# Kernel optimization log

Hardware: AMD Instinct MI355X
Metric: run time of the kernel (lower is better)

Reference implementation:

```python
import jax, jax.numpy as jnp
import numpy as np

N = 50000   # num_nodes
D = 128     # h_dim
R = 32      # num_rels * 2 (forward + inverse relations)
B = 8       # num_bases
E = 600000  # num_edges


def setup_inputs() -> dict:
    key = jax.random.key(0)
    ks = jax.random.split(key, 14)
    s = 1.0 / np.sqrt(D)
    return {
        "h_ids": jnp.arange(N, dtype=jnp.int32),
        "src": jax.random.randint(ks[0], (E,), 0, N),
        "dst": jax.random.randint(ks[1], (E,), 0, N),
        "etype": jax.random.randint(ks[2], (E,), 0, R),
        "norm": jax.random.uniform(ks[3], (E, 1), dtype=jnp.float32),
        "embedding": jax.random.normal(ks[4], (N, D), dtype=jnp.float32) * 0.05,
        "w_comp1": jax.random.normal(ks[5], (R, B), dtype=jnp.float32) * (1.0 / np.sqrt(B)),
        "bases1": jax.random.normal(ks[6], (B, D, D), dtype=jnp.float32) * s,
        "loop_w1": jax.random.normal(ks[7], (D, D), dtype=jnp.float32) * s,
        "bias1": jnp.zeros((D,), dtype=jnp.float32),
        "w_comp2": jax.random.normal(ks[8], (R, B), dtype=jnp.float32) * (1.0 / np.sqrt(B)),
        "bases2": jax.random.normal(ks[9], (B, D, D), dtype=jnp.float32) * s,
        "loop_w2": jax.random.normal(ks[10], (D, D), dtype=jnp.float32) * s,
        "bias2": jnp.zeros((D,), dtype=jnp.float32),
    }


def _rel_graph_conv(h, src, dst, etype, norm, w_comp, bases, loop_w, bias, act):
    # basis decomposition: W[r] = sum_b w_comp[r,b] * bases[b]
    W = jnp.einsum('rb,bio->rio', w_comp, bases)          # [R, D, D]
    # transform every node by every relation weight (dense GEMM)
    all_t = jnp.einsum('ni,rio->nro', h, W)               # [N, R, D]
    # per-edge gather of relation-specific transformed source features
    msg = all_t[src, etype] * norm                        # [E, D]
    # scatter-aggregate messages at destination nodes
    agg = jax.ops.segment_sum(msg, dst, num_segments=h.shape[0])  # [N, D]
    out = agg + h @ loop_w + bias                         # self-loop + bias
    return act(out) if act is not None else out


def reference(h_ids, src, dst, etype, norm, embedding,
              w_comp1, bases1, loop_w1, bias1,
              w_comp2, bases2, loop_w2, bias2):
    # EmbeddingLayer
    h = embedding[h_ids]                                  # [N, D]
    # hidden layer 0: relu activation (idx < num_hidden_layers-1)
    h = _rel_graph_conv(h, src, dst, etype, norm, w_comp1, bases1, loop_w1, bias1, jax.nn.relu)
    # hidden layer 1: no activation (last layer)
    h = _rel_graph_conv(h, src, dst, etype, norm, w_comp2, bases2, loop_w2, bias2, None)
    return h
```

## Files before the change

### kernel.cpp

```cpp
#include <hip/hip_runtime.h>

#define DD 128
#define NB 8
#define KTOT 1152

typedef unsigned int uint_t;
typedef __attribute__((ext_vector_type(8))) _Float16 half8v;
typedef __attribute__((ext_vector_type(2))) _Float16 half2v;
typedef __attribute__((ext_vector_type(4))) float f32x4;

static __device__ __forceinline__ void gld_lds16(const _Float16* g, _Float16* l)
{
  __builtin_amdgcn_global_load_lds(
      (const __attribute__((address_space(1))) void*)g,
      (__attribute__((address_space(3))) void*)l, 16, 0, 0);
}

static __device__ __forceinline__ half2v bc_h2(uint_t u)
{
  union { uint_t u; half2v h; } c; c.u = u; return c.h;
}

static __device__ __forceinline__ float fdot2(uint_t a, uint_t b, float acc)
{
#if __has_builtin(__builtin_amdgcn_fdot2)
  return __builtin_amdgcn_fdot2(bc_h2(a), bc_h2(b), acc, false);
#else
  half2v x = bc_h2(a), y = bc_h2(b);
  return acc + (float)x[0] * (float)y[0] + (float)x[1] * (float)y[1];
#endif
}

__global__ __launch_bounds__(256) void k_prep_w(
    const float* __restrict__ bases1, const float* __restrict__ loopw1,
    const float* __restrict__ bases2, const float* __restrict__ loopw2,
    _Float16* __restrict__ WcA)
{
  int i = blockIdx.x * 256 + threadIdx.x;
  if (i >= 2 * 36 * DD * 32) return;
  int layer = i / (36 * DD * 32);
  int rem   = i % (36 * DD * 32);
  int ks    = rem / (DD * 32);
  int rem2  = rem % (DD * 32);
  int feat  = rem2 / 32;
  int j     = rem2 % 32;
  int k     = ks * 32 + j;
  const float* basesL = layer ? bases2 : bases1;
  const float* loopwL = layer ? loopw2 : loopw1;
  float v;
  if (k < 1024) {
    int kk = k >> 3, b = k & 7;
    v = basesL[((size_t)b * DD + kk) * DD + feat];
  } else {
    v = loopwL[(size_t)(k - 1024) * DD + feat];
  }
  WcA[i] = (_Float16)v;
}

__global__ __launch_bounds__(256) void k_cast(
    const float* __restrict__ h, const int* __restrict__ ids,
    _Float16* __restrict__ hf, int N)
{
  int i = blockIdx.x * 256 + threadIdx.x;
  if (i >= N * (DD / 8)) return;
  int n  = i / (DD / 8);
  int k8 = (i % (DD / 8)) * 8;
  int row = ids ? ids[n] : n;
  const float* hp = h + (size_t)row * DD + k8;
  float4 v0 = *(const float4*)hp;
  float4 v1 = *(const float4*)(hp + 4);
  union { _Float16 e[8]; uint4 q; } p;
  p.e[0]=(_Float16)v0.x; p.e[1]=(_Float16)v0.y; p.e[2]=(_Float16)v0.z; p.e[3]=(_Float16)v0.w;
  p.e[4]=(_Float16)v1.x; p.e[5]=(_Float16)v1.y; p.e[6]=(_Float16)v1.z; p.e[7]=(_Float16)v1.w;
  *(uint4*)&hf[(size_t)n * DD + k8] = p.q;
}

__global__ __launch_bounds__(256) void k_zero(int* __restrict__ p, int n)
{
  int i = blockIdx.x * 256 + threadIdx.x;
  if (i < n) p[i] = 0;
}

__global__ __launch_bounds__(256) void k_hist(
    const int* __restrict__ dst, int* __restrict__ cnt, int E)
{
  int e = blockIdx.x * 256 + threadIdx.x;
  if (e < E) atomicAdd(&cnt[dst[e]], 1);
}

__global__ __launch_bounds__(256) void k_bsum(
    const int* __restrict__ cnt, int* __restrict__ bsum, int N)
{
  __shared__ int s[256];
  int i = blockIdx.x * 256 + threadIdx.x;
  s[threadIdx.x] = (i < N) ? ((cnt[i] + 1) & ~1) : 0;
  __syncthreads();
  for (int off = 128; off > 0; off >>= 1) {
    if (threadIdx.x < off) s[threadIdx.x] += s[threadIdx.x + off];
    __syncthreads();
  }
  if (threadIdx.x == 0) bsum[blockIdx.x] = s[0];
}

__global__ __launch_bounds__(256) void k_scanb(
    const int* __restrict__ bsum, int* __restrict__ boff, int nb)
{
  __shared__ int s[256];
  int t = threadIdx.x;
  int own = (t < nb) ? bsum[t] : 0;
  s[t] = own;
  __syncthreads();
  for (int off = 1; off < 256; off <<= 1) {
    int v = (t >= off) ? s[t - off] : 0;
    __syncthreads();
    s[t] += v;
    __syncthreads();
  }
  if (t < nb) boff[t] = s[t] - own;
}

__global__ __launch_bounds__(256) void k_scan3(
    const int* __restrict__ cnt, const int* __restrict__ boff,
    int* __restrict__ row_start, int* __restrict__ psrc, int N)
{
  __shared__ int s[256];
  int t = threadIdx.x;
  int i = blockIdx.x * 256 + t;
  int c = (i < N) ? cnt[i] : 0;
  int v = (c + 1) & ~1;
  s[t] = v;
  __syncthreads();
  for (int off = 1; off < 256; off <<= 1) {
    int u = (t >= off) ? s[t - off] : 0;
    __syncthreads();
    s[t] += u;
    __syncthreads();
  }
  if (i < N) {
    int rs = boff[blockIdx.x] + s[t] - v;
    row_start[i] = rs;
    if (c & 1) psrc[rs + c] = 0;
  }
}

__global__ __launch_bounds__(256) void k_place(
    const int* __restrict__ dst, const int* __restrict__ src,
    const int* __restrict__ etype, const float* __restrict__ norm,
    const int* __restrict__ row_start, int* __restrict__ cursor,
    int* __restrict__ psrc, int2* __restrict__ en, int E)
{
  int e = blockIdx.x * 256 + threadIdx.x;
  if (e < E) {
    int v = dst[e];
    int slot = row_start[v] + atomicAdd(&cursor[v], 1);
    psrc[slot] = src[e];
    en[slot] = make_int2(etype[e], __float_as_int(norm[e]));
  }
}

__global__ __launch_bounds__(256) void k_payload_pair(
    const int2* __restrict__ en,
    const float* __restrict__ wcomp1, const float* __restrict__ wcomp2,
    _Float16* __restrict__ c1, _Float16* __restrict__ c2, int npair)
{
  int i = blockIdx.x * 256 + threadIdx.x;
  if (i >= npair) return;
  int2 e0 = en[2 * i], e1 = en[2 * i + 1];
  float n0 = __int_as_float(e0.y), n1 = __int_as_float(e1.y);
  const float* w10 = wcomp1 + e0.x * NB;
  const float* w11 = wcomp1 + e1.x * NB;
  const float* w20 = wcomp2 + e0.x * NB;
  const float* w21 = wcomp2 + e1.x * NB;

  union { _Float16 h[16]; uint4 q[2]; } p;
  #pragma unroll
  for (int b = 0; b < NB; b++) {
    p.h[b * 2]     = (_Float16)(w10[b] * n0);
    p.h[b * 2 + 1] = (_Float16)(w11[b] * n1);
  }
  *(uint4*)&c1[(size_t)i * 16]     = p.q[0];
  *(uint4*)&c1[(size_t)i * 16 + 8] = p.q[1];
  #pragma unroll
  for (int b = 0; b < NB; b++) {
    p.h[b * 2]     = (_Float16)(w20[b] * n0);
    p.h[b * 2 + 1] = (_Float16)(w21[b] * n1);
  }
  *(uint4*)&c2[(size_t)i * 16]     = p.q[0];
  *(uint4*)&c2[(size_t)i * 16 + 8] = p.q[1];
}

__global__ __launch_bounds__(256) void k_agg(
    const int* __restrict__ rowst, const int* __restrict__ cnt,
    const int* __restrict__ psrc, const _Float16* __restrict__ cpair,
    const _Float16* __restrict__ hf,
    _Float16* __restrict__ agg, int N)
{
  int v = blockIdx.x * 4 + (threadIdx.x >> 6);
  if (v >= N) return;
  int lane = threadIdx.x & 63;
  const uint_t* hf32 = (const uint_t*)hf;
  const int beg = rowst[v];
  const int npairs = (cnt[v] + 1) >> 1;
  const uint_t* cp = (const uint_t*)cpair + (size_t)(beg >> 1) * 8;
  const int* ps = psrc + beg;

  float ax[NB] = {}, ay[NB] = {};
  int i = 0;
  for (; i + 4 <= npairs; i += 4) {
    uint_t u[8], lo[4], hi[4];
    #pragma unroll
    for (int q = 0; q < 8; q++)
      u[q] = hf32[(size_t)ps[2*i + q] * 64 + lane];
    #pragma unroll
    for (int q = 0; q < 4; q++) {
      lo[q] = __builtin_amdgcn_perm(u[2*q], u[2*q+1], 0x01000504);
      hi[q] = __builtin_amdgcn_perm(u[2*q], u[2*q+1], 0x03020706);
    }
    #pragma unroll
    for (int b = 0; b < NB; b++) {
      #pragma unroll
      for (int q = 0; q < 4; q++) {
        uint_t cc = cp[(size_t)(i + q) * 8 + b];
        ax[b] = fdot2(cc, lo[q], ax[b]);
        ay[b] = fdot2(cc, hi[q], ay[b]);
      }
    }
  }
  for (; i + 2 <= npairs; i += 2) {
    int s0 = ps[2*i + 0], s1 = ps[2*i + 1];
    int s2 = ps[2*i + 2], s3 = ps[2*i + 3];
    uint_t u0 = hf32[(size_t)s0 * 64 + lane];
    uint_t u1 = hf32[(size_t)s1 * 64 + lane];
    uint_t u2 = hf32[(size_t)s2 * 64 + lane];
    uint_t u3 = hf32[(size_t)s3 * 64 + lane];
    uint_t lo01 = __builtin_amdgcn_perm(u0, u1, 0x01000504);
    uint_t hi01 = __builtin_amdgcn_perm(u0, u1, 0x03020706);
    uint_t lo23 = __builtin_amdgcn_perm(u2, u3, 0x01000504);
    uint_t hi23 = __builtin_amdgcn_perm(u2, u3, 0x03020706);
    #pragma unroll
    for (int b = 0; b < NB; b++) {
      uint_t ca = cp[(size_t)i * 8 + b];
      uint_t cb = cp[(size_t)(i + 1) * 8 + b];
      ax[b] = fdot2(ca, lo01, ax[b]);
      ay[b] = fdot2(ca, hi01, ay[b]);
      ax[b] = fdot2(cb, lo23, ax[b]);
      ay[b] = fdot2(cb, hi23, ay[b]);
    }
  }
  if (i < npairs) {
    int s0 = ps[2*i + 0], s1 = ps[2*i + 1];
    uint_t u0 = hf32[(size_t)s0 * 64 + lane];
    uint_t u1 = hf32[(size_t)s1 * 64 + lane];
    uint_t lo01 = __builtin_amdgcn_perm(u0, u1, 0x01000504);
    uint_t hi01 = __builtin_amdgcn_perm(u0, u1, 0x03020706);
    #pragma unroll
    for (int b = 0; b < NB; b++) {
      uint_t ca = cp[(size_t)i * 8 + b];
      ax[b] = fdot2(ca, lo01, ax[b]);
      ay[b] = fdot2(ca, hi01, ay[b]);
    }
  }

  union { _Float16 e[8]; uint4 q; } p0, p1;
  #pragma unroll
  for (int b = 0; b < NB; b++) { p0.e[b] = (_Float16)ax[b]; p1.e[b] = (_Float16)ay[b]; }
  uint4* dstp = (uint4*)&agg[(size_t)v * 1024 + lane * 16];
  dstp[0] = p0.q;
  dstp[1] = p1.q;
}

template <int LAYER>
__global__ __launch_bounds__(256) void k_mm(
    const _Float16* __restrict__ agg,
    const _Float16* __restrict__ hf,
    const _Float16* __restrict__ WcA,
    const float* __restrict__ bias,
    float* __restrict__ outf, _Float16* __restrict__ outh, int N)
{
  __shared__ _Float16 sB[2][2048];

  const int n0   = blockIdx.x * 32;
  const int wv   = threadIdx.x >> 6;
  const int lane = threadIdx.x & 63;
  const int l15  = lane & 15, l4 = lane >> 4;

  int nodeS = n0 + (lane & 31); if (nodeS >= N) nodeS = N - 1;
  const int ksl = 2 * wv + (lane >> 5);

  f32x4 acc[2][2];
  #pragma unroll
  for (int a = 0; a < 2; a++)
    #pragma unroll
    for (int b = 0; b < 2; b++) acc[a][b] = (f32x4)0.f;

  const int fbase = wv * 32 + l15;
  const int koff  = l4 * 8;

  auto STAGE = [&](int buf, int t) {
    const _Float16* g;
    if (t < 16) g = &agg[(size_t)nodeS * 1024 + t * 64 + ksl * 8];
    else        g = &hf [(size_t)nodeS * DD   + (t - 16) * 64 + ksl * 8];
    gld_lds16(g, &sB[buf][2 * wv * 256]);
  };

  auto COMPUTE = [&](int buf, int t) {
    #pragma unroll
    for (int sub = 0; sub < 2; sub++) {
      const int ks = 2 * t + sub;
      half8v af0 = *(const half8v*)&WcA[((size_t)ks * DD + fbase     ) * 32 + koff];
      half8v af1 = *(const half8v*)&WcA[((size_t)ks * DD + fbase + 16) * 32 + koff];
      half8v bf0 = *(const half8v*)&sB[buf][(sub * 4 + l4) * 256 + l15 * 8];
      half8v bf1 = *(const half8v*)&sB[buf][(sub * 4 + l4) * 256 + (16 + l15) * 8];
      acc[0][0] = __builtin_amdgcn_mfma_f32_16x16x32_f16(af0, bf0, acc[0][0], 0, 0, 0);
      acc[0][1] = __builtin_amdgcn_mfma_f32_16x16x32_f16(af0, bf1, acc[0][1], 0, 0, 0);
      acc[1][0] = __builtin_amdgcn_mfma_f32_16x16x32_f16(af1, bf0, acc[1][0], 0, 0, 0);
      acc[1][1] = __builtin_amdgcn_mfma_f32_16x16x32_f16(af1, bf1, acc[1][1], 0, 0, 0);
    }
  };

  STAGE(0, 0);
  __syncthreads();
  int cur = 0;
  for (int t = 0; t < 17; t++) {
    STAGE(cur ^ 1, t + 1);
    COMPUTE(cur, t);
    __syncthreads();
    cur ^= 1;
  }
  COMPUTE(cur, 17);

  #pragma unroll
  for (int mf = 0; mf < 2; mf++)
    #pragma unroll
    for (int nf = 0; nf < 2; nf++) {
      int n = n0 + nf * 16 + l15;
      if (n >= N) continue;
      int feat = wv * 32 + mf * 16 + l4 * 4;
      if (LAYER == 1) {
        union { _Float16 e[4]; uint2 q; } p;
        #pragma unroll
        for (int r = 0; r < 4; r++)
          p.e[r] = (_Float16)fmaxf(acc[mf][nf][r] + bias[feat + r], 0.f);
        *(uint2*)&outh[(size_t)n * DD + feat] = p.q;
      } else {
        float4 o;
        o.x = acc[mf][nf][0] + bias[feat + 0];
        o.y = acc[mf][nf][1] + bias[feat + 1];
        o.z = acc[mf][nf][2] + bias[feat + 2];
        o.w = acc[mf][nf][3] + bias[feat + 3];
        *(float4*)&outf[(size_t)n * DD + feat] = o;
      }
    }
}

extern "C" void kernel_launch(void* const* d_in, const int* in_sizes, int n_in,
                              void* d_out, int out_size, void* d_ws, size_t ws_size,
                              hipStream_t stream)
{
  const int*   h_ids     = (const int*)d_in[0];
  const int*   src       = (const int*)d_in[1];
  const int*   dst       = (const int*)d_in[2];
  const int*   etype     = (const int*)d_in[3];
  const float* norm      = (const float*)d_in[4];
  const float* embedding = (const float*)d_in[5];
  const float* w_comp1   = (const float*)d_in[6];
  const float* bases1    = (const float*)d_in[7];
  const float* loop_w1   = (const float*)d_in[8];
  const float* bias1     = (const float*)d_in[9];
  const float* w_comp2   = (const float*)d_in[10];
  const float* bases2    = (const float*)d_in[11];
  const float* loop_w2   = (const float*)d_in[12];
  const float* bias2     = (const float*)d_in[13];

  const int N = in_sizes[0];
  const int E = in_sizes[1];
  const int S = (E + N) & ~1;
  const int NPAIR = S >> 1;
  const int NBLK = (N + 255) / 256;

  char* base = (char*)d_ws;
  size_t off = 0;
  auto alloc = [&](size_t bytes) -> char* {
    char* p = base + off;
    off += (bytes + 255) & ~(size_t)255;
    return p;
  };
  _Float16* agg  = (_Float16*)alloc((size_t)N * 1024 * 2);
  _Float16* hfp  = (_Float16*)alloc((size_t)N * DD * 2);
  _Float16* h1h  = (_Float16*)alloc((size_t)N * DD * 2);
  _Float16* WcA  = (_Float16*)alloc((size_t)2 * 36 * DD * 32 * 2);
  int*      cnt    = (int*)   alloc((size_t)2 * N * 4);
  int*      cursor = cnt + N;
  int2*     en     = (int2*)  alloc((size_t)S * 8);
  int*      rowst  = (int*)   alloc((size_t)N * 4);
  int*      bsum   = (int*)   alloc(256 * 4);
  int*      boff   = (int*)   alloc(256 * 4);
  int*      psrc   = (int*)   alloc((size_t)S * 4);
  _Float16* c1     = (_Float16*)alloc((size_t)S * 8 * 2);
  _Float16* c2     = (_Float16*)alloc((size_t)S * 8 * 2);
  float*    out    = (float*)d_out;

  int zn = (int)(((char*)(en + S) - (char*)cnt) / 4);
  k_zero <<<(zn + 255) / 256, 256, 0, stream>>>(cnt, zn);
  k_hist <<<(E + 255) / 256, 256, 0, stream>>>(dst, cnt, E);
  k_bsum <<<NBLK, 256, 0, stream>>>(cnt, bsum, N);
  k_scanb<<<1, 256, 0, stream>>>(bsum, boff, NBLK);
  k_scan3<<<NBLK, 256, 0, stream>>>(cnt, boff, rowst, psrc, N);
  k_place<<<(E + 255) / 256, 256, 0, stream>>>(dst, src, etype, norm,
                                               rowst, cursor, psrc, en, E);
  k_payload_pair<<<(NPAIR + 255) / 256, 256, 0, stream>>>(
      en, w_comp1, w_comp2, c1, c2, NPAIR);

  k_prep_w<<<(2 * 36 * DD * 32 + 255) / 256, 256, 0, stream>>>(bases1, loop_w1, bases2, loop_w2, WcA);

  dim3 gmm((N + 31) / 32);
  int gagg = (N + 3) / 4;

  k_cast<<<(N * (DD / 8) + 255) / 256, 256, 0, stream>>>(embedding, h_ids, hfp, N);
  k_agg<<<gagg, 256, 0, stream>>>(rowst, cnt, psrc, c1, hfp, agg, N);
  k_mm<1><<<gmm, 256, 0, stream>>>(agg, hfp, WcA, bias1, nullptr, h1h, N);

  k_agg<<<gagg, 256, 0, stream>>>(rowst, cnt, psrc, c2, h1h, agg, N);
  k_mm<2><<<gmm, 256, 0, stream>>>(agg, h1h, WcA + (size_t)36 * DD * 32, bias2, out, nullptr, N);
}
```

Measured before the change: 289.4 us.

## Fuse per-basis aggregation and MFMA projection into one kernel per layer

Merges the edge-aggregation kernel and the MFMA GEMM kernel so each block of 16 nodes aggregates its per-basis features straight into a swizzled LDS tile, appends the self-loop features, and then runs the 36-step MFMA reduction from LDS. This removes the N x 1024 fp16 intermediate buffer round trip through global memory and two launches. In exchange, tiles shrink from 32 to 16 nodes, the weight fragments are reloaded per 16-node block, double-buffered async staging is dropped, and each block's GEMM waits on its slowest node's aggregation.

```diff
diff --git a/kernel.cpp b/kernel.cpp
--- a/kernel.cpp
+++ b/kernel.cpp
@@ -8,13 +8,6 @@
 typedef __attribute__((ext_vector_type(8))) _Float16 half8v;
 typedef __attribute__((ext_vector_type(2))) _Float16 half2v;
 typedef __attribute__((ext_vector_type(4))) float f32x4;
-
-static __device__ __forceinline__ void gld_lds16(const _Float16* g, _Float16* l)
-{
-  __builtin_amdgcn_global_load_lds(
-      (const __attribute__((address_space(1))) void*)g,
-      (__attribute__((address_space(3))) void*)l, 16, 0, 0);
-}
 
 static __device__ __forceinline__ half2v bc_h2(uint_t u)
 {
@@ -189,168 +182,134 @@
   *(uint4*)&c2[(size_t)i * 16 + 8] = p.q[1];
 }
 
-__global__ __launch_bounds__(256) void k_agg(
+template <int LAYER>
+__global__ __launch_bounds__(256) void k_fused(
     const int* __restrict__ rowst, const int* __restrict__ cnt,
     const int* __restrict__ psrc, const _Float16* __restrict__ cpair,
-    const _Float16* __restrict__ hf,
-    _Float16* __restrict__ agg, int N)
-{
-  int v = blockIdx.x * 4 + (threadIdx.x >> 6);
-  if (v >= N) return;
-  int lane = threadIdx.x & 63;
-  const uint_t* hf32 = (const uint_t*)hf;
-  const int beg = rowst[v];
-  const int npairs = (cnt[v] + 1) >> 1;
-  const uint_t* cp = (const uint_t*)cpair + (size_t)(beg >> 1) * 8;
-  const int* ps = psrc + beg;
-
-  float ax[NB] = {}, ay[NB] = {};
-  int i = 0;
-  for (; i + 4 <= npairs; i += 4) {
-    uint_t u[8], lo[4], hi[4];
-    #pragma unroll
-    for (int q = 0; q < 8; q++)
-      u[q] = hf32[(size_t)ps[2*i + q] * 64 + lane];
-    #pragma unroll
-    for (int q = 0; q < 4; q++) {
-      lo[q] = __builtin_amdgcn_perm(u[2*q], u[2*q+1], 0x01000504);
-      hi[q] = __builtin_amdgcn_perm(u[2*q], u[2*q+1], 0x03020706);
-    }
-    #pragma unroll
-    for (int b = 0; b < NB; b++) {
-      #pragma unroll
-      for (int q = 0; q < 4; q++) {
-        uint_t cc = cp[(size_t)(i + q) * 8 + b];
-        ax[b] = fdot2(cc, lo[q], ax[b]);
-        ay[b] = fdot2(cc, hi[q], ay[b]);
-      }
-    }
-  }
-  for (; i + 2 <= npairs; i += 2) {
-    int s0 = ps[2*i + 0], s1 = ps[2*i + 1];
-    int s2 = ps[2*i + 2], s3 = ps[2*i + 3];
-    uint_t u0 = hf32[(size_t)s0 * 64 + lane];
-    uint_t u1 = hf32[(size_t)s1 * 64 + lane];
-    uint_t u2 = hf32[(size_t)s2 * 64 + lane];
-    uint_t u3 = hf32[(size_t)s3 * 64 + lane];
-    uint_t lo01 = __builtin_amdgcn_perm(u0, u1, 0x01000504);
-    uint_t hi01 = __builtin_amdgcn_perm(u0, u1, 0x03020706);
-    uint_t lo23 = __builtin_amdgcn_perm(u2, u3, 0x01000504);
-    uint_t hi23 = __builtin_amdgcn_perm(u2, u3, 0x03020706);
-    #pragma unroll
-    for (int b = 0; b < NB; b++) {
-      uint_t ca = cp[(size_t)i * 8 + b];
-      uint_t cb = cp[(size_t)(i + 1) * 8 + b];
-      ax[b] = fdot2(ca, lo01, ax[b]);
-      ay[b] = fdot2(ca, hi01, ay[b]);
-      ax[b] = fdot2(cb, lo23, ax[b]);
-      ay[b] = fdot2(cb, hi23, ay[b]);
-    }
-  }
-  if (i < npairs) {
-    int s0 = ps[2*i + 0], s1 = ps[2*i + 1];
-    uint_t u0 = hf32[(size_t)s0 * 64 + lane];
-    uint_t u1 = hf32[(size_t)s1 * 64 + lane];
-    uint_t lo01 = __builtin_amdgcn_perm(u0, u1, 0x01000504);
-    uint_t hi01 = __builtin_amdgcn_perm(u0, u1, 0x03020706);
-    #pragma unroll
-    for (int b = 0; b < NB; b++) {
-      uint_t ca = cp[(size_t)i * 8 + b];
-      ax[b] = fdot2(ca, lo01, ax[b]);
-      ay[b] = fdot2(ca, hi01, ay[b]);
-    }
-  }
-
-  union { _Float16 e[8]; uint4 q; } p0, p1;
-  #pragma unroll
-  for (int b = 0; b < NB; b++) { p0.e[b] = (_Float16)ax[b]; p1.e[b] = (_Float16)ay[b]; }
-  uint4* dstp = (uint4*)&agg[(size_t)v * 1024 + lane * 16];
-  dstp[0] = p0.q;
-  dstp[1] = p1.q;
-}
-
-template <int LAYER>
-__global__ __launch_bounds__(256) void k_mm(
-    const _Float16* __restrict__ agg,
     const _Float16* __restrict__ hf,
     const _Float16* __restrict__ WcA,
     const float* __restrict__ bias,
     float* __restrict__ outf, _Float16* __restrict__ outh, int N)
 {
-  __shared__ _Float16 sB[2][2048];
-
-  const int n0   = blockIdx.x * 32;
+  __shared__ _Float16 sB[144 * 16 * 8];
+
+  const int n0   = blockIdx.x * 16;
   const int wv   = threadIdx.x >> 6;
   const int lane = threadIdx.x & 63;
   const int l15  = lane & 15, l4 = lane >> 4;
-
-  int nodeS = n0 + (lane & 31); if (nodeS >= N) nodeS = N - 1;
-  const int ksl = 2 * wv + (lane >> 5);
-
-  f32x4 acc[2][2];
-  #pragma unroll
-  for (int a = 0; a < 2; a++)
+  const uint_t* hf32 = (const uint_t*)hf;
+
+  for (int r = wv; r < 16; r += 4) {
+    int v = n0 + r;
+    if (v >= N) continue;
+    const int beg = rowst[v];
+    const int npairs = (cnt[v] + 1) >> 1;
+    const uint_t* cp = (const uint_t*)cpair + (size_t)(beg >> 1) * 8;
+    const int* ps = psrc + beg;
+
+    float ax[NB] = {}, ay[NB] = {};
+    int i = 0;
+    for (; i + 4 <= npairs; i += 4) {
+      uint_t u[8], lo[4], hi[4];
+      #pragma unroll
+      for (int q = 0; q < 8; q++)
+        u[q] = hf32[(size_t)ps[2*i + q] * 64 + lane];
+      #pragma unroll
+      for (int q = 0; q < 4; q++) {
+        lo[q] = __builtin_amdgcn_perm(u[2*q], u[2*q+1], 0x01000504);
+        hi[q] = __builtin_amdgcn_perm(u[2*q], u[2*q+1], 0x03020706);
+      }
+      #pragma unroll
+      for (int b = 0; b < NB; b++) {
+        #pragma unroll
+        for (int q = 0; q < 4; q++) {
+          uint_t cc = cp[(size_t)(i + q) * 8 + b];
+          ax[b] = fdot2(cc, lo[q], ax[b]);
+          ay[b] = fdot2(cc, hi[q], ay[b]);
+        }
+      }
+    }
+    for (; i + 2 <= npairs; i += 2) {
+      uint_t u0 = hf32[(size_t)ps[2*i + 0] * 64 + lane];
+      uint_t u1 = hf32[(size_t)ps[2*i + 1] * 64 + lane];
+      uint_t u2 = hf32[(size_t)ps[2*i + 2] * 64 + lane];
+      uint_t u3 = hf32[(size_t)ps[2*i + 3] * 64 + lane];
+      uint_t lo01 = __builtin_amdgcn_perm(u0, u1, 0x01000504);
+      uint_t hi01 = __builtin_amdgcn_perm(u0, u1, 0x03020706);
+      uint_t lo23 = __builtin_amdgcn_perm(u2, u3, 0x01000504);
+      uint_t hi23 = __builtin_amdgcn_perm(u2, u3, 0x03020706);
+      #pragma unroll
+      for (int b = 0; b < NB; b++) {
+        uint_t ca = cp[(size_t)i * 8 + b];
+        uint_t cb = cp[(size_t)(i + 1) * 8 + b];
+        ax[b] = fdot2(ca, lo01, ax[b]);
+        ay[b] = fdot2(ca, hi01, ay[b]);
+        ax[b] = fdot2(cb, lo23, ax[b]);
+        ay[b] = fdot2(cb, hi23, ay[b]);
+      }
+    }
+    if (i < npairs) {
+      uint_t u0 = hf32[(size_t)ps[2*i + 0] * 64 + lane];
+      uint_t u1 = hf32[(size_t)ps[2*i + 1] * 64 + lane];
+      uint_t lo01 = __builtin_amdgcn_perm(u0, u1, 0x01000504);
+      uint_t hi01 = __builtin_amdgcn_perm(u0, u1, 0x03020706);
+      #pragma unroll
+      for (int b = 0; b < NB; b++) {
+        uint_t ca = cp[(size_t)i * 8 + b];
+        ax[b] = fdot2(ca, lo01, ax[b]);
+        ay[b] = fdot2(ca, hi01, ay[b]);
+      }
+    }
+
+    union { _Float16 e[8]; uint4 q; } p0, p1;
     #pragma unroll
-    for (int b = 0; b < 2; b++) acc[a][b] = (f32x4)0.f;
-
+    for (int b = 0; b < NB; b++) { p0.e[b] = (_Float16)ax[b]; p1.e[b] = (_Float16)ay[b]; }
+    int c0 = 2 * lane, c1 = 2 * lane + 1;
+    *(uint4*)&sB[(c0 * 16 + ((r + c0) & 15)) * 8] = p0.q;
+    *(uint4*)&sB[(c1 * 16 + ((r + c1) & 15)) * 8] = p1.q;
+    uint_t hv = hf32[(size_t)v * 64 + lane];
+    int ch = 128 + (lane >> 5) * 8 + ((lane & 31) >> 2);
+    int jb = ((2 * lane) & 7) * 2;
+    *(uint_t*)((char*)sB + (ch * 16 + ((r + ch) & 15)) * 16 + jb) = hv;
+  }
+  __syncthreads();
+
+  f32x4 acc[2];
+  acc[0] = (f32x4)0.f; acc[1] = (f32x4)0.f;
   const int fbase = wv * 32 + l15;
   const int koff  = l4 * 8;
 
-  auto STAGE = [&](int buf, int t) {
-    const _Float16* g;
-    if (t < 16) g = &agg[(size_t)nodeS * 1024 + t * 64 + ksl * 8];
-    else        g = &hf [(size_t)nodeS * DD   + (t - 16) * 64 + ksl * 8];
-    gld_lds16(g, &sB[buf][2 * wv * 256]);
-  };
-
-  auto COMPUTE = [&](int buf, int t) {
+  #pragma unroll 6
+  for (int ks = 0; ks < 36; ks++) {
+    half8v af0 = *(const half8v*)&WcA[((size_t)ks * DD + fbase     ) * 32 + koff];
+    half8v af1 = *(const half8v*)&WcA[((size_t)ks * DD + fbase + 16) * 32 + koff];
+    int c = (ks >> 1) * 8 + (ks & 1) * 4 + l4;
+    half8v bf = *(const half8v*)&sB[(c * 16 + ((l15 + c) & 15)) * 8];
+    acc[0] = __builtin_amdgcn_mfma_f32_16x16x32_f16(af0, bf, acc[0], 0, 0, 0);
+    acc[1] = __builtin_amdgcn_mfma_f32_16x16x32_f16(af1, bf, acc[1], 0, 0, 0);
+  }
+
+  int n = n0 + l15;
+  if (n < N) {
     #pragma unroll
-    for (int sub = 0; sub < 2; sub++) {
-      const int ks = 2 * t + sub;
-      half8v af0 = *(const half8v*)&WcA[((size_t)ks * DD + fbase     ) * 32 + koff];
-      half8v af1 = *(const half8v*)&WcA[((size_t)ks * DD + fbase + 16) * 32 + koff];
-      half8v bf0 = *(const half8v*)&sB[buf][(sub * 4 + l4) * 256 + l15 * 8];
-      half8v bf1 = *(const half8v*)&sB[buf][(sub * 4 + l4) * 256 + (16 + l15) * 8];
-      acc[0][0] = __builtin_amdgcn_mfma_f32_16x16x32_f16(af0, bf0, acc[0][0], 0, 0, 0);
-      acc[0][1] = __builtin_amdgcn_mfma_f32_16x16x32_f16(af0, bf1, acc[0][1], 0, 0, 0);
-      acc[1][0] = __builtin_amdgcn_mfma_f32_16x16x32_f16(af1, bf0, acc[1][0], 0, 0, 0);
-      acc[1][1] = __builtin_amdgcn_mfma_f32_16x16x32_f16(af1, bf1, acc[1][1], 0, 0, 0);
-    }
-  };
-
-  STAGE(0, 0);
-  __syncthreads();
-  int cur = 0;
-  for (int t = 0; t < 17; t++) {
-    STAGE(cur ^ 1, t + 1);
-    COMPUTE(cur, t);
-    __syncthreads();
-    cur ^= 1;
-  }
-  COMPUTE(cur, 17);
-
-  #pragma unroll
-  for (int mf = 0; mf < 2; mf++)
-    #pragma unroll
-    for (int nf = 0; nf < 2; nf++) {
-      int n = n0 + nf * 16 + l15;
-      if (n >= N) continue;
+    for (int mf = 0; mf < 2; mf++) {
       int feat = wv * 32 + mf * 16 + l4 * 4;
       if (LAYER == 1) {
         union { _Float16 e[4]; uint2 q; } p;
         #pragma unroll
-        for (int r = 0; r < 4; r++)
-          p.e[r] = (_Float16)fmaxf(acc[mf][nf][r] + bias[feat + r], 0.f);
+        for (int rr = 0; rr < 4; rr++)
+          p.e[rr] = (_Float16)fmaxf(acc[mf][rr] + bias[feat + rr], 0.f);
         *(uint2*)&outh[(size_t)n * DD + feat] = p.q;
       } else {
         float4 o;
-        o.x = acc[mf][nf][0] + bias[feat + 0];
-        o.y = acc[mf][nf][1] + bias[feat + 1];
-        o.z = acc[mf][nf][2] + bias[feat + 2];
-        o.w = acc[mf][nf][3] + bias[feat + 3];
+        o.x = acc[mf][0] + bias[feat + 0];
+        o.y = acc[mf][1] + bias[feat + 1];
+        o.z = acc[mf][2] + bias[feat + 2];
+        o.w = acc[mf][3] + bias[feat + 3];
         *(float4*)&outf[(size_t)n * DD + feat] = o;
       }
     }
+  }
 }
 
 extern "C" void kernel_launch(void* const* d_in, const int* in_sizes, int n_in,
@@ -385,7 +344,6 @@
     off += (bytes + 255) & ~(size_t)255;
     return p;
   };
-  _Float16* agg  = (_Float16*)alloc((size_t)N * 1024 * 2);
   _Float16* hfp  = (_Float16*)alloc((size_t)N * DD * 2);
   _Float16* h1h  = (_Float16*)alloc((size_t)N * DD * 2);
   _Float16* WcA  = (_Float16*)alloc((size_t)2 * 36 * DD * 32 * 2);
@@ -413,13 +371,11 @@
 
   k_prep_w<<<(2 * 36 * DD * 32 + 255) / 256, 256, 0, stream>>>(bases1, loop_w1, bases2, loop_w2, WcA);
 
-  dim3 gmm((N + 31) / 32);
-  int gagg = (N + 3) / 4;
+  dim3 gf((N + 15) / 16);
 
   k_cast<<<(N * (DD / 8) + 255) / 256, 256, 0, stream>>>(embedding, h_ids, hfp, N);
-  k_agg<<<gagg, 256, 0, stream>>>(rowst, cnt, psrc, c1, hfp, agg, N);
-  k_mm<1><<<gmm, 256, 0, stream>>>(agg, hfp, WcA, bias1, nullptr, h1h, N);
-
-  k_agg<<<gagg, 256, 0, stream>>>(rowst, cnt, psrc, c2, h1h, agg, N);
-  k_mm<2><<<gmm, 256, 0, stream>>>(agg, h1h, WcA + (size_t)36 * DD * 32, bias2, out, nullptr, N);
-}
+  k_fused<1><<<gf, 256, 0, stream>>>(rowst, cnt, psrc, c1, hfp, WcA, bias1,
+                                     nullptr, h1h, N);
+  k_fused<2><<<gf, 256, 0, stream>>>(rowst, cnt, psrc, c2, h1h,
+                                     WcA + (size_t)36 * DD * 32, bias2, out, nullptr, N);
+}
```

Result: no change. 291.8 us (+0.8%).

## Widen MFMA node tile to 64 and record histogram slots to drop second atomic

Applied to the files above, without the earlier changes.

The GEMM kernel now processes 64 nodes per block instead of 32, with a 2x4 MFMA accumulator grid. Each weight fragment loaded from global memory is therefore reused across twice as many node columns, halving weight traffic per node. Separately, the histogram kernel saves each edge's atomic return value as its within-row slot, so the placement kernel no longer needs a second atomic pass over a cursor array. The costs are more accumulator registers and twice the LDS per block, which may lower occupancy, plus an extra E-sized int buffer.

```diff
diff --git a/kernel.cpp b/kernel.cpp
--- a/kernel.cpp
+++ b/kernel.cpp
@@ -82,10 +82,11 @@
 }
 
 __global__ __launch_bounds__(256) void k_hist(
-    const int* __restrict__ dst, int* __restrict__ cnt, int E)
+    const int* __restrict__ dst, int* __restrict__ cnt,
+    int* __restrict__ slotin, int E)
 {
   int e = blockIdx.x * 256 + threadIdx.x;
-  if (e < E) atomicAdd(&cnt[dst[e]], 1);
+  if (e < E) slotin[e] = atomicAdd(&cnt[dst[e]], 1);
 }
 
 __global__ __launch_bounds__(256) void k_bsum(
@@ -146,13 +147,12 @@
 __global__ __launch_bounds__(256) void k_place(
     const int* __restrict__ dst, const int* __restrict__ src,
     const int* __restrict__ etype, const float* __restrict__ norm,
-    const int* __restrict__ row_start, int* __restrict__ cursor,
+    const int* __restrict__ row_start, const int* __restrict__ slotin,
     int* __restrict__ psrc, int2* __restrict__ en, int E)
 {
   int e = blockIdx.x * 256 + threadIdx.x;
   if (e < E) {
-    int v = dst[e];
-    int slot = row_start[v] + atomicAdd(&cursor[v], 1);
+    int slot = row_start[dst[e]] + slotin[e];
     psrc[slot] = src[e];
     en[slot] = make_int2(etype[e], __float_as_int(norm[e]));
   }
@@ -227,12 +227,10 @@
     }
   }
   for (; i + 2 <= npairs; i += 2) {
-    int s0 = ps[2*i + 0], s1 = ps[2*i + 1];
-    int s2 = ps[2*i + 2], s3 = ps[2*i + 3];
-    uint_t u0 = hf32[(size_t)s0 * 64 + lane];
-    uint_t u1 = hf32[(size_t)s1 * 64 + lane];
-    uint_t u2 = hf32[(size_t)s2 * 64 + lane];
-    uint_t u3 = hf32[(size_t)s3 * 64 + lane];
+    uint_t u0 = hf32[(size_t)ps[2*i + 0] * 64 + lane];
+    uint_t u1 = hf32[(size_t)ps[2*i + 1] * 64 + lane];
+    uint_t u2 = hf32[(size_t)ps[2*i + 2] * 64 + lane];
+    uint_t u3 = hf32[(size_t)ps[2*i + 3] * 64 + lane];
     uint_t lo01 = __builtin_amdgcn_perm(u0, u1, 0x01000504);
     uint_t hi01 = __builtin_amdgcn_perm(u0, u1, 0x03020706);
     uint_t lo23 = __builtin_amdgcn_perm(u2, u3, 0x01000504);
@@ -248,9 +246,8 @@
     }
   }
   if (i < npairs) {
-    int s0 = ps[2*i + 0], s1 = ps[2*i + 1];
-    uint_t u0 = hf32[(size_t)s0 * 64 + lane];
-    uint_t u1 = hf32[(size_t)s1 * 64 + lane];
+    uint_t u0 = hf32[(size_t)ps[2*i + 0] * 64 + lane];
+    uint_t u1 = hf32[(size_t)ps[2*i + 1] * 64 + lane];
     uint_t lo01 = __builtin_amdgcn_perm(u0, u1, 0x01000504);
     uint_t hi01 = __builtin_amdgcn_perm(u0, u1, 0x03020706);
     #pragma unroll
@@ -277,44 +274,53 @@
     const float* __restrict__ bias,
     float* __restrict__ outf, _Float16* __restrict__ outh, int N)
 {
-  __shared__ _Float16 sB[2][2048];
-
-  const int n0   = blockIdx.x * 32;
+  __shared__ _Float16 sB[2][4096];
+
+  const int n0   = blockIdx.x * 64;
   const int wv   = threadIdx.x >> 6;
   const int lane = threadIdx.x & 63;
   const int l15  = lane & 15, l4 = lane >> 4;
 
-  int nodeS = n0 + (lane & 31); if (nodeS >= N) nodeS = N - 1;
-  const int ksl = 2 * wv + (lane >> 5);
-
-  f32x4 acc[2][2];
+  int nodeL = n0 + lane; if (nodeL >= N) nodeL = N - 1;
+
+  f32x4 acc[2][4];
   #pragma unroll
   for (int a = 0; a < 2; a++)
     #pragma unroll
-    for (int b = 0; b < 2; b++) acc[a][b] = (f32x4)0.f;
+    for (int b = 0; b < 4; b++) acc[a][b] = (f32x4)0.f;
 
   const int fbase = wv * 32 + l15;
   const int koff  = l4 * 8;
 
   auto STAGE = [&](int buf, int t) {
-    const _Float16* g;
-    if (t < 16) g = &agg[(size_t)nodeS * 1024 + t * 64 + ksl * 8];
-    else        g = &hf [(size_t)nodeS * DD   + (t - 16) * 64 + ksl * 8];
-    gld_lds16(g, &sB[buf][2 * wv * 256]);
+    const _Float16 *g0, *g1;
+    if (t < 16) {
+      g0 = &agg[(size_t)nodeL * 1024 + (2 * t)     * 32 + wv * 8];
+      g1 = &agg[(size_t)nodeL * 1024 + (2 * t + 1) * 32 + wv * 8];
+    } else {
+      g0 = &hf[(size_t)nodeL * DD + (2 * t - 32) * 32 + wv * 8];
+      g1 = &hf[(size_t)nodeL * DD + (2 * t - 31) * 32 + wv * 8];
+    }
+    gld_lds16(g0, &sB[buf][ wv      * 512]);
+    gld_lds16(g1, &sB[buf][(wv + 4) * 512]);
   };
 
   auto COMPUTE = [&](int buf, int t) {
     #pragma unroll
     for (int sub = 0; sub < 2; sub++) {
       const int ks = 2 * t + sub;
-      half8v af0 = *(const half8v*)&WcA[((size_t)ks * DD + fbase     ) * 32 + koff];
-      half8v af1 = *(const half8v*)&WcA[((size_t)ks * DD + fbase + 16) * 32 + koff];
-      half8v bf0 = *(const half8v*)&sB[buf][(sub * 4 + l4) * 256 + l15 * 8];
-      half8v bf1 = *(const half8v*)&sB[buf][(sub * 4 + l4) * 256 + (16 + l15) * 8];
-      acc[0][0] = __builtin_amdgcn_mfma_f32_16x16x32_f16(af0, bf0, acc[0][0], 0, 0, 0);
-      acc[0][1] = __builtin_amdgcn_mfma_f32_16x16x32_f16(af0, bf1, acc[0][1], 0, 0, 0);
-      acc[1][0] = __builtin_amdgcn_mfma_f32_16x16x32_f16(af1, bf0, acc[1][0], 0, 0, 0);
-      acc[1][1] = __builtin_amdgcn_mfma_f32_16x16x32_f16(af1, bf1, acc[1][1], 0, 0, 0);
+      half8v af[2], bfr[4];
+      #pragma unroll
+      for (int mf = 0; mf < 2; mf++)
+        af[mf] = *(const half8v*)&WcA[((size_t)ks * DD + fbase + mf * 16) * 32 + koff];
+      #pragma unroll
+      for (int nf = 0; nf < 4; nf++)
+        bfr[nf] = *(const half8v*)&sB[buf][(l4 + sub * 4) * 512 + (nf * 16 + l15) * 8];
+      #pragma unroll
+      for (int mf = 0; mf < 2; mf++)
+        #pragma unroll
+        for (int nf = 0; nf < 4; nf++)
+          acc[mf][nf] = __builtin_amdgcn_mfma_f32_16x16x32_f16(af[mf], bfr[nf], acc[mf][nf], 0, 0, 0);
     }
   };
 
@@ -332,7 +338,7 @@
   #pragma unroll
   for (int mf = 0; mf < 2; mf++)
     #pragma unroll
-    for (int nf = 0; nf < 2; nf++) {
+    for (int nf = 0; nf < 4; nf++) {
       int n = n0 + nf * 16 + l15;
       if (n >= N) continue;
       int feat = wv * 32 + mf * 16 + l4 * 4;
@@ -389,12 +395,12 @@
   _Float16* hfp  = (_Float16*)alloc((size_t)N * DD * 2);
   _Float16* h1h  = (_Float16*)alloc((size_t)N * DD * 2);
   _Float16* WcA  = (_Float16*)alloc((size_t)2 * 36 * DD * 32 * 2);
-  int*      cnt    = (int*)   alloc((size_t)2 * N * 4);
-  int*      cursor = cnt + N;
+  int*      cnt    = (int*)   alloc((size_t)N * 4);
   int2*     en     = (int2*)  alloc((size_t)S * 8);
   int*      rowst  = (int*)   alloc((size_t)N * 4);
   int*      bsum   = (int*)   alloc(256 * 4);
   int*      boff   = (int*)   alloc(256 * 4);
+  int*      slotin = (int*)   alloc((size_t)E * 4);
   int*      psrc   = (int*)   alloc((size_t)S * 4);
   _Float16* c1     = (_Float16*)alloc((size_t)S * 8 * 2);
   _Float16* c2     = (_Float16*)alloc((size_t)S * 8 * 2);
@@ -402,18 +408,18 @@
 
   int zn = (int)(((char*)(en + S) - (char*)cnt) / 4);
   k_zero <<<(zn + 255) / 256, 256, 0, stream>>>(cnt, zn);
-  k_hist <<<(E + 255) / 256, 256, 0, stream>>>(dst, cnt, E);
+  k_hist <<<(E + 255) / 256, 256, 0, stream>>>(dst, cnt, slotin, E);
   k_bsum <<<NBLK, 256, 0, stream>>>(cnt, bsum, N);
   k_scanb<<<1, 256, 0, stream>>>(bsum, boff, NBLK);
   k_scan3<<<NBLK, 256, 0, stream>>>(cnt, boff, rowst, psrc, N);
   k_place<<<(E + 255) / 256, 256, 0, stream>>>(dst, src, etype, norm,
-                                               rowst, cursor, psrc, en, E);
+                                               rowst, slotin, psrc, en, E);
   k_payload_pair<<<(NPAIR + 255) / 256, 256, 0, stream>>>(
       en, w_comp1, w_comp2, c1, c2, NPAIR);
 
   k_prep_w<<<(2 * 36 * DD * 32 + 255) / 256, 256, 0, stream>>>(bases1, loop_w1, bases2, loop_w2, WcA);
 
-  dim3 gmm((N + 31) / 32);
+  dim3 gmm((N + 63) / 64);
   int gagg = (N + 3) / 4;
 
   k_cast<<<(N * (DD / 8) + 255) / 256, 256, 0, stream>>>(embedding, h_ids, hfp, N);
```

Result: faster. 255.7 us (-11.6%).
